# Kernel optimization log

Hardware: AMD Instinct MI355X
Metric: run time of the kernel (lower is better)

## Reference

```python
import jax, jax.numpy as jnp
import numpy as np

N, E, DIN, H, C, L = 100000, 1600000, 128, 128, 40, 4
EPS = 1e-5  # BatchNorm1d default eps


def _bn(x, g, b):
    # training-mode batchnorm over node dim, biased variance (PyTorch normalizes
    # the batch with biased var in forward)
    m = jnp.mean(x, axis=0)
    v = jnp.var(x, axis=0)
    return g * (x - m) * jax.lax.rsqrt(v + EPS) + b


def _sage(h, src, dst, Wl_i, bl_i, Wr_i):
    # PyG SAGEConv (aggr='mean', root_weight=True): lin_l(mean_j x_j) + lin_r(x_i)
    msg = h[src]                                             # [E, H]
    s = jax.ops.segment_sum(msg, dst, num_segments=N)        # [N, H]
    cnt = jax.ops.segment_sum(jnp.ones((E, 1), h.dtype), dst, num_segments=N)
    agg = s / jnp.maximum(cnt, 1.0)
    return agg @ Wl_i + bl_i + h @ Wr_i


def setup_inputs() -> dict:
    key = jax.random.key(0)
    ks = jax.random.split(key, 14)
    s = 0.05
    x = jax.random.normal(ks[0], (N, DIN), dtype=jnp.float32)
    edge_index = jax.random.randint(ks[1], (2, E), 0, N)
    return {
        "x": x,
        "W_in": jax.random.normal(ks[2], (DIN, H), dtype=jnp.float32) * s,
        "b_in": jnp.zeros((H,), jnp.float32),
        "g_in": jnp.ones((H,), jnp.float32),
        "beta_in": jnp.zeros((H,), jnp.float32),
        "Wl": jax.random.normal(ks[3], (L, H, H), dtype=jnp.float32) * s,
        "bl": jnp.zeros((L, H), jnp.float32),
        "Wr": jax.random.normal(ks[4], (L, H, H), dtype=jnp.float32) * s,
        "g_bn": jnp.ones((L, H), jnp.float32),
        "b_bn": jnp.zeros((L, H), jnp.float32),
        "W_out": jax.random.normal(ks[5], (H, C), dtype=jnp.float32) * s,
        "b_out": jnp.zeros((C,), jnp.float32),
        "edge_index": edge_index,
    }


def reference(x, W_in, b_in, g_in, beta_in, Wl, bl, Wr, g_bn, b_bn, W_out, b_out, edge_index):
    src, dst = edge_index[0], edge_index[1]
    h = jax.nn.relu(_bn(x @ W_in + b_in, g_in, beta_in))  # dropout p=0.0 -> identity
    for i in range(L):
        h = _sage(h, src, dst, Wl[i], bl[i], Wr[i])
        if i < L - 1:
            h = jax.nn.relu(_bn(h, g_bn[i], b_bn[i]))
    return h @ W_out + b_out
```

## Files before the change

### kernel.cpp

```cpp
#include <hip/hip_runtime.h>

#define N_NODES 100000
#define N_EDGES 1600000
#define HD 128
#define NLAYERS 4
#define COUT 40
#define BN_EPS 1e-5f
#define NBUCK 782
#define BUCK_CAP 3072
constexpr int GB = (N_NODES + 127) / 128;

typedef _Float16 half8 __attribute__((ext_vector_type(8)));
typedef float floatx4 __attribute__((ext_vector_type(4)));

__global__ void prep_kernel(const float* __restrict__ W_in,
                            const float* __restrict__ Wl,
                            const float* __restrict__ Wr,
                            const float* __restrict__ W_out,
                            _Float16* __restrict__ Wt_in,
                            _Float16* __restrict__ Wt_cat,
                            _Float16* __restrict__ Wt_out)
{
    int tid = blockIdx.x * blockDim.x + threadIdx.x;
    int stride = gridDim.x * blockDim.x;
    for (int idx = tid; idx < 128 * 128; idx += stride) {
        int n = idx >> 7, k = idx & 127;
        Wt_in[idx] = (_Float16)W_in[k * 128 + n];
    }
    for (int idx = tid; idx < 4 * 128 * 256; idx += stride) {
        int i = idx >> 15;
        int r = idx & 32767;
        int n = r >> 8, k = r & 255;
        Wt_cat[idx] = (_Float16)((k < 128) ? Wl[i * 16384 + k * 128 + n]
                                           : Wr[i * 16384 + (k - 128) * 128 + n]);
    }
    for (int idx = tid; idx < 48 * 128; idx += stride) {
        int n = idx >> 7, k = idx & 127;
        Wt_out[idx] = (n < COUT) ? (_Float16)W_out[k * COUT + n] : (_Float16)0.f;
    }
}

__global__ __launch_bounds__(256) void bucket_hist_kernel(const int* __restrict__ edst,
                                                          int* __restrict__ bcnt) {
    __shared__ int h[NBUCK];
    for (int b = threadIdx.x; b < NBUCK; b += 256) h[b] = 0;
    __syncthreads();
    int tid = blockIdx.x * 256 + threadIdx.x;
    int stride = gridDim.x * 256;
    for (int e = tid; e < N_EDGES; e += stride)
        atomicAdd(&h[edst[e] >> 7], 1);
    __syncthreads();
    for (int b = threadIdx.x; b < NBUCK; b += 256)
        if (h[b]) atomicAdd(&bcnt[b], h[b]);
}

__global__ void bucket_scan_kernel(const int* __restrict__ bcnt,
                                   int* __restrict__ bbase, int* __restrict__ bcur) {
    int lane = threadIdx.x;
    int run = 0;
    for (int base = 0; base < NBUCK; base += 64) {
        int i = base + lane;
        int orig = (i < NBUCK) ? bcnt[i] : 0;
        int v = orig;
        #pragma unroll
        for (int off = 1; off < 64; off <<= 1) {
            int t = __shfl_up(v, off);
            if (lane >= off) v += t;
        }
        int total = __shfl(v, 63);
        int excl = v - orig + run;
        if (i < NBUCK) { bbase[i] = excl; bcur[i] = excl; }
        run += total;
    }
    if (lane == 0) bbase[NBUCK] = run;
}

#define SCAT_T 16
__global__ __launch_bounds__(512) void bucket_scatter_kernel(const int* __restrict__ esrc,
                                                             const int* __restrict__ edst,
                                                             int* __restrict__ bcur,
                                                             int* __restrict__ bedges) {
    __shared__ int cnt[NBUCK], gpos[NBUCK];
    long base = (long)blockIdx.x * (512 * SCAT_T);
    for (int b = threadIdx.x; b < NBUCK; b += 512) cnt[b] = 0;
    __syncthreads();
    int srcs[SCAT_T], locs[SCAT_T], rnk[SCAT_T], bks[SCAT_T];
    #pragma unroll
    for (int j = 0; j < SCAT_T; ++j) {
        long e = base + j * 512 + threadIdx.x;
        if (e < N_EDGES) {
            int d = edst[e];
            srcs[j] = esrc[e];
            bks[j] = d >> 7;
            locs[j] = d & 127;
            rnk[j] = atomicAdd(&cnt[bks[j]], 1);
        } else bks[j] = -1;
    }
    __syncthreads();
    for (int b = threadIdx.x; b < NBUCK; b += 512) {
        int c = cnt[b];
        gpos[b] = c ? atomicAdd(&bcur[b], c) : 0;
    }
    __syncthreads();
    #pragma unroll
    for (int j = 0; j < SCAT_T; ++j)
        if (bks[j] >= 0)
            bedges[gpos[bks[j]] + rnk[j]] = (locs[j] << 17) | srcs[j];
}

__global__ __launch_bounds__(256) void bucket_sort_kernel(const int* __restrict__ bedges,
                                                          const int* __restrict__ bbase,
                                                          int* __restrict__ rs,
                                                          int* __restrict__ ssrc) {
    __shared__ int lsrc[BUCK_CAP];
    __shared__ int h[128], hin[128], lcur[128];
    int b = blockIdx.x;
    int s = bbase[b];
    int n = bbase[b + 1] - s;
    if (n > BUCK_CAP) n = BUCK_CAP;
    if (threadIdx.x < 128) h[threadIdx.x] = 0;
    __syncthreads();
    for (int i = threadIdx.x; i < n; i += 256) {
        int v = bedges[s + i];
        lsrc[i] = v;
        atomicAdd(&h[v >> 17], 1);
    }
    __syncthreads();
    if (threadIdx.x < 128) hin[threadIdx.x] = h[threadIdx.x];
    __syncthreads();
    #pragma unroll
    for (int off = 1; off < 128; off <<= 1) {
        int t = 0;
        if (threadIdx.x < 128 && (int)threadIdx.x >= off) t = h[threadIdx.x - off];
        __syncthreads();
        if (threadIdx.x < 128) h[threadIdx.x] += t;
        __syncthreads();
    }
    if (threadIdx.x < 128) {
        int excl = h[threadIdx.x] - hin[threadIdx.x];
        lcur[threadIdx.x] = excl;
        int node = b * 128 + threadIdx.x;
        if (node < N_NODES) rs[node] = s + excl;
    }
    if (b == NBUCK - 1 && threadIdx.x == 0) rs[N_NODES] = bbase[NBUCK];
    __syncthreads();
    for (int i = threadIdx.x; i < n; i += 256) {
        int v = lsrc[i];
        int r = atomicAdd(&lcur[v >> 17], 1);
        ssrc[s + r] = v & 0x1FFFF;
    }
}

__global__ __launch_bounds__(256) void aggregate_kernel(const _Float16* __restrict__ H,
                                                        const int* __restrict__ rs,
                                                        const int* __restrict__ ssrc,
                                                        _Float16* __restrict__ AGG) {
    int wid = (blockIdx.x * 256 + threadIdx.x) >> 6;
    int lane = threadIdx.x & 63;
    int grp = lane >> 4, l16 = lane & 15;
    int dst = wid * 4 + grp;
    int e0 = rs[dst], e1 = rs[dst + 1];
    int deg = e1 - e0;

    half8 acca = {0, 0, 0, 0, 0, 0, 0, 0};
    half8 accb = {0, 0, 0, 0, 0, 0, 0, 0};
    const _Float16* __restrict__ Hc = H + l16 * 8;

    int e = e0;
    for (; e + 4 <= e1; e += 4) {
        int s0 = ssrc[e], s1 = ssrc[e + 1], s2 = ssrc[e + 2], s3 = ssrc[e + 3];
        half8 v0 = *(const half8*)(Hc + (long)s0 * HD);
        half8 v1 = *(const half8*)(Hc + (long)s1 * HD);
        half8 v2 = *(const half8*)(Hc + (long)s2 * HD);
        half8 v3 = *(const half8*)(Hc + (long)s3 * HD);
        acca += v0 + v1;
        accb += v2 + v3;
    }
    for (; e < e1; ++e) {
        half8 v0 = *(const half8*)(Hc + (long)ssrc[e] * HD);
        acca += v0;
    }
    half8 acc = acca + accb;
    _Float16 inv = (_Float16)(1.f / (float)max(deg, 1));
    acc *= inv;
    *(half8*)(AGG + (long)dst * HD + l16 * 8) = acc;
}

template <int CT, int KS, bool HAS_A1, bool A_F32, bool OUT_F32, bool STATS>
__global__ __launch_bounds__(256, 2) void gemm_kernel(const void* __restrict__ A0v,
                                                      const _Float16* __restrict__ A1,
                                                      const _Float16* __restrict__ Wt,
                                                      const float* __restrict__ bias,
                                                      void* __restrict__ Yv,
                                                      int out_stride, int ncols,
                                                      float* __restrict__ gstats) {
    constexpr int K = KS * 32;
    constexpr int KSC = (KS > 4) ? 4 : KS;
    __shared__ _Float16 bsm[KSC * 32 * CT * 16];
    int wave = threadIdx.x >> 6;
    int lane = threadIdx.x & 63;
    int quad = lane >> 4;
    int l16 = lane & 15;
    int row_base = (blockIdx.x * 4 + wave) * 32;
    bool active = row_base < N_NODES;

    floatx4 acc[2][CT];
    #pragma unroll
    for (int rt = 0; rt < 2; ++rt)
        #pragma unroll
        for (int c = 0; c < CT; ++c)
            acc[rt][c] = (floatx4){0.f, 0.f, 0.f, 0.f};

    for (int ch = 0; ch < KS; ch += KSC) {
        if (ch) __syncthreads();
        for (int i = threadIdx.x; i < KSC * CT * 64; i += 256) {
            int n = i % (CT * 16);
            int ko = i / (CT * 16);
            half8 v = *(const half8*)(Wt + n * K + (ch * 4 + ko) * 8);
            int slot = (((ko >> 2) * CT + (n >> 4)) * 4 + (ko & 3)) * 16 + (n & 15);
            *(half8*)(bsm + slot * 8) = v;
        }
        __syncthreads();
        if (active) {
            #pragma unroll
            for (int s2 = 0; s2 < KSC; ++s2) {
                int s = ch + s2;
                int kk = s * 32 + quad * 8;
                half8 afrag[2];
                #pragma unroll
                for (int rt = 0; rt < 2; ++rt) {
                    int r = row_base + rt * 16 + l16;
                    if (r > N_NODES - 1) r = N_NODES - 1;
                    if (A_F32) {
                        const float* p = (const float*)A0v + (long)r * 128 + kk;
                        floatx4 f0 = *(const floatx4*)p;
                        floatx4 f1 = *(const floatx4*)(p + 4);
                        #pragma unroll
                        for (int j = 0; j < 4; ++j) {
                            afrag[rt][j]     = (_Float16)f0[j];
                            afrag[rt][4 + j] = (_Float16)f1[j];
                        }
                    } else {
                        const _Float16* p;
                        if (HAS_A1 && kk >= 128) p = A1 + (long)r * 128 + (kk - 128);
                        else                     p = (const _Float16*)A0v + (long)r * 128 + kk;
                        afrag[rt] = *(const half8*)p;
                    }
                }
                #pragma unroll
                for (int c = 0; c < CT; ++c) {
                    half8 bfrag = *(const half8*)(bsm + ((s2 * CT + c) * 64 + lane) * 8);
                    #pragma unroll
                    for (int rt = 0; rt < 2; ++rt)
                        acc[rt][c] = __builtin_amdgcn_mfma_f32_16x16x32_f16(afrag[rt], bfrag, acc[rt][c], 0, 0, 0);
                }
            }
        }
    }

    float* lsum = (float*)bsm;
    float* lsq  = lsum + 128;
    if (STATS) {
        __syncthreads();
        if (threadIdx.x < 128) { lsum[threadIdx.x] = 0.f; lsq[threadIdx.x] = 0.f; }
        __syncthreads();
    } else {
        if (!active) return;
    }

    #pragma unroll
    for (int c = 0; c < CT; ++c) {
        int col = c * 16 + l16;
        float s_c = 0.f, q_c = 0.f;
        if (active && col < ncols) {
            float bv = bias[col];
            #pragma unroll
            for (int rt = 0; rt < 2; ++rt) {
                #pragma unroll
                for (int i = 0; i < 4; ++i) {
                    int r = row_base + rt * 16 + quad * 4 + i;
                    if (r < N_NODES) {
                        float v = acc[rt][c][i] + bv;
                        if (OUT_F32) ((float*)Yv)[(long)r * out_stride + col] = v;
                        else         ((_Float16*)Yv)[(long)r * out_stride + col] = (_Float16)v;
                        if (STATS) { s_c += v; q_c += v * v; }
                    }
                }
            }
        }
        if (STATS) {
            s_c += __shfl_xor(s_c, 16); s_c += __shfl_xor(s_c, 32);
            q_c += __shfl_xor(q_c, 16); q_c += __shfl_xor(q_c, 32);
            if (lane < 16 && active) {
                atomicAdd(&lsum[col], s_c);
                atomicAdd(&lsq[col], q_c);
            }
        }
    }

    if (STATS) {
        __syncthreads();
        if (threadIdx.x < 128) {
            atomicAdd(&gstats[threadIdx.x], lsum[threadIdx.x]);
            atomicAdd(&gstats[128 + threadIdx.x], lsq[threadIdx.x]);
        }
    }
}

__global__ __launch_bounds__(256) void bn_apply_kernel(const _Float16* __restrict__ Y,
                                                       const float* __restrict__ gstats,
                                                       const float* __restrict__ g,
                                                       const float* __restrict__ b,
                                                       _Float16* __restrict__ H) {
    __shared__ float sc[128], sh[128];
    if (threadIdx.x < 128) {
        int col = threadIdx.x;
        float m = gstats[col] * (1.f / (float)N_NODES);
        float v = gstats[128 + col] * (1.f / (float)N_NODES) - m * m;
        float s = g[col] * rsqrtf(v + BN_EPS);
        sc[col] = s;
        sh[col] = b[col] - m * s;
    }
    __syncthreads();
    long total = (long)N_NODES * HD / 8;
    for (long t = (long)blockIdx.x * blockDim.x + threadIdx.x; t < total;
         t += (long)gridDim.x * blockDim.x) {
        long base = t * 8;
        int col0 = (int)(base & 127);
        half8 in = *(const half8*)(Y + base);
        half8 outv;
        #pragma unroll
        for (int j = 0; j < 8; ++j) {
            float v = (float)in[j];
            float r = v * sc[col0 + j] + sh[col0 + j];
            outv[j] = (_Float16)fmaxf(r, 0.f);
        }
        *(half8*)(H + base) = outv;
    }
}

extern "C" void kernel_launch(void* const* d_in, const int* in_sizes, int n_in,
                              void* d_out, int out_size, void* d_ws, size_t ws_size,
                              hipStream_t stream) {
    (void)in_sizes; (void)n_in; (void)out_size; (void)ws_size;
    const float* x       = (const float*)d_in[0];
    const float* W_in    = (const float*)d_in[1];
    const float* b_in    = (const float*)d_in[2];
    const float* g_in    = (const float*)d_in[3];
    const float* beta_in = (const float*)d_in[4];
    const float* Wl      = (const float*)d_in[5];
    const float* bl      = (const float*)d_in[6];
    const float* Wr      = (const float*)d_in[7];
    const float* g_bn    = (const float*)d_in[8];
    const float* b_bn    = (const float*)d_in[9];
    const float* W_out   = (const float*)d_in[10];
    const float* b_out   = (const float*)d_in[11];
    const int*   ei      = (const int*)d_in[12];
    const int* esrc = ei;
    const int* edst = ei + N_EDGES;
    float* out = (float*)d_out;

    char* w = (char*)d_ws;
    auto alloc = [&](size_t bytes) -> char* {
        char* p = w; w += (bytes + 255) & ~(size_t)255; return p;
    };
    int* rs           = (int*)alloc((N_NODES + 1) * sizeof(int));
    int* bcnt         = (int*)alloc((NBUCK + 1) * sizeof(int));
    int* bbase        = (int*)alloc((NBUCK + 1) * sizeof(int));
    int* bcur         = (int*)alloc(NBUCK * sizeof(int));
    int* ssrc         = (int*)alloc(N_EDGES * sizeof(int));
    _Float16* Wt_in   = (_Float16*)alloc(128 * 128 * 2);
    _Float16* Wt_cat  = (_Float16*)alloc(4 * 128 * 256 * 2);
    _Float16* Wt_out  = (_Float16*)alloc(48 * 128 * 2);
    _Float16* hbuf    = (_Float16*)alloc((size_t)N_NODES * HD * 2);
    _Float16* agg     = (_Float16*)alloc((size_t)N_NODES * HD * 2);
    _Float16* ybuf    = (_Float16*)alloc((size_t)N_NODES * HD * 2);
    float* gstats     = (float*)alloc(4 * 256 * 4);
    int* bedges       = (int*)agg;

    hipMemsetAsync(bcnt, 0, (NBUCK + 1) * sizeof(int), stream);
    hipMemsetAsync(gstats, 0, 4 * 256 * 4, stream);
    prep_kernel<<<256, 256, 0, stream>>>(W_in, Wl, Wr, W_out, Wt_in, Wt_cat, Wt_out);
    bucket_hist_kernel<<<64, 256, 0, stream>>>(edst, bcnt);
    bucket_scan_kernel<<<1, 64, 0, stream>>>(bcnt, bbase, bcur);
    bucket_scatter_kernel<<<(N_EDGES + 8191) / 8192, 512, 0, stream>>>(esrc, edst, bcur, bedges);
    bucket_sort_kernel<<<NBUCK, 256, 0, stream>>>(bedges, bbase, rs, ssrc);

    gemm_kernel<8, 4, false, true, false, true><<<GB, 256, 0, stream>>>(
        x, nullptr, Wt_in, b_in, ybuf, HD, HD, gstats);
    bn_apply_kernel<<<1600, 256, 0, stream>>>(ybuf, gstats, g_in, beta_in, hbuf);

    for (int i = 0; i < NLAYERS; ++i) {
        aggregate_kernel<<<N_NODES / 16, 256, 0, stream>>>(hbuf, rs, ssrc, agg);
        if (i < NLAYERS - 1) {
            float* gs = gstats + (i + 1) * 256;
            gemm_kernel<8, 8, true, false, false, true><<<GB, 256, 0, stream>>>(
                agg, hbuf, Wt_cat + i * 128 * 256, bl + i * 128, ybuf, HD, HD, gs);
            bn_apply_kernel<<<1600, 256, 0, stream>>>(ybuf, gs, g_bn + i * 128, b_bn + i * 128, hbuf);
        } else {
            gemm_kernel<8, 8, true, false, false, false><<<GB, 256, 0, stream>>>(
                agg, hbuf, Wt_cat + i * 128 * 256, bl + i * 128, ybuf, HD, HD, nullptr);
        }
    }

    gemm_kernel<3, 4, false, false, true, false><<<GB, 256, 0, stream>>>(
        ybuf, nullptr, Wt_out, b_out, out, COUT, COUT, nullptr);
}
```

Baseline: 651.0 us.

## Fuse BatchNorm+ReLU into aggregate gather and GEMM A-operand loads

Removes the separate bn_apply pass by storing pre-normalization outputs and applying per-column scale/shift plus ReLU inside the aggregate kernel's gathers and the GEMM's root-feature fragment loads. This drops a full read-and-write pass over the 100000x128 fp16 activations per layer. In exchange, normalization is recomputed for every gathered edge (16x per node on average), and the scale/shift are held in fp16 rather than fp32. It also ping-pongs two activation buffers so the GEMM can read the previous layer's output while writing the next.

```diff
diff --git a/kernel.cpp b/kernel.cpp
--- a/kernel.cpp
+++ b/kernel.cpp
@@ -12,6 +12,12 @@
 
 typedef _Float16 half8 __attribute__((ext_vector_type(8)));
 typedef float floatx4 __attribute__((ext_vector_type(4)));
+
+__device__ __forceinline__ half8 bnrelu8(half8 v, half8 s, half8 h) {
+    half8 t = s * v + h;
+    half8 z = {0, 0, 0, 0, 0, 0, 0, 0};
+    return __builtin_elementwise_max(t, z);
+}
 
 __global__ void prep_kernel(const float* __restrict__ W_in,
                             const float* __restrict__ Wl,
@@ -151,10 +157,24 @@
     }
 }
 
-__global__ __launch_bounds__(256) void aggregate_kernel(const _Float16* __restrict__ H,
+__global__ __launch_bounds__(256) void aggregate_kernel(const _Float16* __restrict__ Y,
                                                         const int* __restrict__ rs,
                                                         const int* __restrict__ ssrc,
+                                                        const float* __restrict__ gstats,
+                                                        const float* __restrict__ g,
+                                                        const float* __restrict__ b,
                                                         _Float16* __restrict__ AGG) {
+    __shared__ _Float16 sc16[128], sh16[128];
+    if (threadIdx.x < 128) {
+        int col = threadIdx.x;
+        float m = gstats[col] * (1.f / (float)N_NODES);
+        float v = gstats[128 + col] * (1.f / (float)N_NODES) - m * m;
+        float s = g[col] * rsqrtf(v + BN_EPS);
+        sc16[col] = (_Float16)s;
+        sh16[col] = (_Float16)(b[col] - m * s);
+    }
+    __syncthreads();
+
     int wid = (blockIdx.x * 256 + threadIdx.x) >> 6;
     int lane = threadIdx.x & 63;
     int grp = lane >> 4, l16 = lane & 15;
@@ -162,23 +182,25 @@
     int e0 = rs[dst], e1 = rs[dst + 1];
     int deg = e1 - e0;
 
+    half8 scv = *(const half8*)(sc16 + l16 * 8);
+    half8 shv = *(const half8*)(sh16 + l16 * 8);
     half8 acca = {0, 0, 0, 0, 0, 0, 0, 0};
     half8 accb = {0, 0, 0, 0, 0, 0, 0, 0};
-    const _Float16* __restrict__ Hc = H + l16 * 8;
+    const _Float16* __restrict__ Yc = Y + l16 * 8;
 
     int e = e0;
     for (; e + 4 <= e1; e += 4) {
         int s0 = ssrc[e], s1 = ssrc[e + 1], s2 = ssrc[e + 2], s3 = ssrc[e + 3];
-        half8 v0 = *(const half8*)(Hc + (long)s0 * HD);
-        half8 v1 = *(const half8*)(Hc + (long)s1 * HD);
-        half8 v2 = *(const half8*)(Hc + (long)s2 * HD);
-        half8 v3 = *(const half8*)(Hc + (long)s3 * HD);
-        acca += v0 + v1;
-        accb += v2 + v3;
+        half8 v0 = *(const half8*)(Yc + (long)s0 * HD);
+        half8 v1 = *(const half8*)(Yc + (long)s1 * HD);
+        half8 v2 = *(const half8*)(Yc + (long)s2 * HD);
+        half8 v3 = *(const half8*)(Yc + (long)s3 * HD);
+        acca += bnrelu8(v0, scv, shv) + bnrelu8(v1, scv, shv);
+        accb += bnrelu8(v2, scv, shv) + bnrelu8(v3, scv, shv);
     }
     for (; e < e1; ++e) {
-        half8 v0 = *(const half8*)(Hc + (long)ssrc[e] * HD);
-        acca += v0;
+        half8 v0 = *(const half8*)(Yc + (long)ssrc[e] * HD);
+        acca += bnrelu8(v0, scv, shv);
     }
     half8 acc = acca + accb;
     _Float16 inv = (_Float16)(1.f / (float)max(deg, 1));
@@ -186,23 +208,38 @@
     *(half8*)(AGG + (long)dst * HD + l16 * 8) = acc;
 }
 
-template <int CT, int KS, bool HAS_A1, bool A_F32, bool OUT_F32, bool STATS>
+template <int CT, int KS, bool HAS_A1, bool A_F32, bool OUT_F32, bool STATS, bool BN_A1>
 __global__ __launch_bounds__(256, 2) void gemm_kernel(const void* __restrict__ A0v,
                                                       const _Float16* __restrict__ A1,
                                                       const _Float16* __restrict__ Wt,
                                                       const float* __restrict__ bias,
                                                       void* __restrict__ Yv,
                                                       int out_stride, int ncols,
-                                                      float* __restrict__ gstats) {
+                                                      float* __restrict__ gstats_out,
+                                                      const float* __restrict__ bn_stats,
+                                                      const float* __restrict__ bn_g,
+                                                      const float* __restrict__ bn_b) {
     constexpr int K = KS * 32;
     constexpr int KSC = (KS > 4) ? 4 : KS;
     __shared__ _Float16 bsm[KSC * 32 * CT * 16];
+    __shared__ _Float16 a1sc[128], a1sh[128];
     int wave = threadIdx.x >> 6;
     int lane = threadIdx.x & 63;
     int quad = lane >> 4;
     int l16 = lane & 15;
     int row_base = (blockIdx.x * 4 + wave) * 32;
     bool active = row_base < N_NODES;
+
+    if (BN_A1) {
+        if (threadIdx.x < 128) {
+            int col = threadIdx.x;
+            float m = bn_stats[col] * (1.f / (float)N_NODES);
+            float v = bn_stats[128 + col] * (1.f / (float)N_NODES) - m * m;
+            float s = bn_g[col] * rsqrtf(v + BN_EPS);
+            a1sc[col] = (_Float16)s;
+            a1sh[col] = (_Float16)(bn_b[col] - m * s);
+        }
+    }
 
     floatx4 acc[2][CT];
     #pragma unroll
@@ -226,6 +263,7 @@
             for (int s2 = 0; s2 < KSC; ++s2) {
                 int s = ch + s2;
                 int kk = s * 32 + quad * 8;
+                bool fromA1 = HAS_A1 && (kk >= 128);
                 half8 afrag[2];
                 #pragma unroll
                 for (int rt = 0; rt < 2; ++rt) {
@@ -242,9 +280,14 @@
                         }
                     } else {
                         const _Float16* p;
-                        if (HAS_A1 && kk >= 128) p = A1 + (long)r * 128 + (kk - 128);
-                        else                     p = (const _Float16*)A0v + (long)r * 128 + kk;
+                        if (fromA1) p = A1 + (long)r * 128 + (kk - 128);
+                        else        p = (const _Float16*)A0v + (long)r * 128 + kk;
                         afrag[rt] = *(const half8*)p;
+                        if (BN_A1 && fromA1) {
+                            half8 s8 = *(const half8*)(a1sc + (kk - 128));
+                            half8 h8 = *(const half8*)(a1sh + (kk - 128));
+                            afrag[rt] = bnrelu8(afrag[rt], s8, h8);
+                        }
                     }
                 }
                 #pragma unroll
@@ -301,41 +344,9 @@
     if (STATS) {
         __syncthreads();
         if (threadIdx.x < 128) {
-            atomicAdd(&gstats[threadIdx.x], lsum[threadIdx.x]);
-            atomicAdd(&gstats[128 + threadIdx.x], lsq[threadIdx.x]);
-        }
-    }
-}
-
-__global__ __launch_bounds__(256) void bn_apply_kernel(const _Float16* __restrict__ Y,
-                                                       const float* __restrict__ gstats,
-                                                       const float* __restrict__ g,
-                                                       const float* __restrict__ b,
-                                                       _Float16* __restrict__ H) {
-    __shared__ float sc[128], sh[128];
-    if (threadIdx.x < 128) {
-        int col = threadIdx.x;
-        float m = gstats[col] * (1.f / (float)N_NODES);
-        float v = gstats[128 + col] * (1.f / (float)N_NODES) - m * m;
-        float s = g[col] * rsqrtf(v + BN_EPS);
-        sc[col] = s;
-        sh[col] = b[col] - m * s;
-    }
-    __syncthreads();
-    long total = (long)N_NODES * HD / 8;
-    for (long t = (long)blockIdx.x * blockDim.x + threadIdx.x; t < total;
-         t += (long)gridDim.x * blockDim.x) {
-        long base = t * 8;
-        int col0 = (int)(base & 127);
-        half8 in = *(const half8*)(Y + base);
-        half8 outv;
-        #pragma unroll
-        for (int j = 0; j < 8; ++j) {
-            float v = (float)in[j];
-            float r = v * sc[col0 + j] + sh[col0 + j];
-            outv[j] = (_Float16)fmaxf(r, 0.f);
-        }
-        *(half8*)(H + base) = outv;
+            atomicAdd(&gstats_out[threadIdx.x], lsum[threadIdx.x]);
+            atomicAdd(&gstats_out[128 + threadIdx.x], lsq[threadIdx.x]);
+        }
     }
 }
 
@@ -372,9 +383,9 @@
     _Float16* Wt_in   = (_Float16*)alloc(128 * 128 * 2);
     _Float16* Wt_cat  = (_Float16*)alloc(4 * 128 * 256 * 2);
     _Float16* Wt_out  = (_Float16*)alloc(48 * 128 * 2);
-    _Float16* hbuf    = (_Float16*)alloc((size_t)N_NODES * HD * 2);
+    _Float16* ybufA   = (_Float16*)alloc((size_t)N_NODES * HD * 2);
+    _Float16* ybufB   = (_Float16*)alloc((size_t)N_NODES * HD * 2);
     _Float16* agg     = (_Float16*)alloc((size_t)N_NODES * HD * 2);
-    _Float16* ybuf    = (_Float16*)alloc((size_t)N_NODES * HD * 2);
     float* gstats     = (float*)alloc(4 * 256 * 4);
     int* bedges       = (int*)agg;
 
@@ -386,23 +397,28 @@
     bucket_scatter_kernel<<<(N_EDGES + 8191) / 8192, 512, 0, stream>>>(esrc, edst, bcur, bedges);
     bucket_sort_kernel<<<NBUCK, 256, 0, stream>>>(bedges, bbase, rs, ssrc);
 
-    gemm_kernel<8, 4, false, true, false, true><<<GB, 256, 0, stream>>>(
-        x, nullptr, Wt_in, b_in, ybuf, HD, HD, gstats);
-    bn_apply_kernel<<<1600, 256, 0, stream>>>(ybuf, gstats, g_in, beta_in, hbuf);
-
+    gemm_kernel<8, 4, false, true, false, true, false><<<GB, 256, 0, stream>>>(
+        x, nullptr, Wt_in, b_in, ybufA, HD, HD, gstats, nullptr, nullptr, nullptr);
+
+    _Float16* cur = ybufA;
+    _Float16* nxt = ybufB;
     for (int i = 0; i < NLAYERS; ++i) {
-        aggregate_kernel<<<N_NODES / 16, 256, 0, stream>>>(hbuf, rs, ssrc, agg);
+        const float* gs   = gstats + i * 256;
+        const float* bn_g = (i == 0) ? g_in    : g_bn + (i - 1) * 128;
+        const float* bn_b = (i == 0) ? beta_in : b_bn + (i - 1) * 128;
+        aggregate_kernel<<<N_NODES / 16, 256, 0, stream>>>(cur, rs, ssrc, gs, bn_g, bn_b, agg);
         if (i < NLAYERS - 1) {
-            float* gs = gstats + (i + 1) * 256;
-            gemm_kernel<8, 8, true, false, false, true><<<GB, 256, 0, stream>>>(
-                agg, hbuf, Wt_cat + i * 128 * 256, bl + i * 128, ybuf, HD, HD, gs);
-            bn_apply_kernel<<<1600, 256, 0, stream>>>(ybuf, gs, g_bn + i * 128, b_bn + i * 128, hbuf);
+            gemm_kernel<8, 8, true, false, false, true, true><<<GB, 256, 0, stream>>>(
+                agg, cur, Wt_cat + i * 128 * 256, bl + i * 128, nxt, HD, HD,
+                gstats + (i + 1) * 256, gs, bn_g, bn_b);
         } else {
-            gemm_kernel<8, 8, true, false, false, false><<<GB, 256, 0, stream>>>(
-                agg, hbuf, Wt_cat + i * 128 * 256, bl + i * 128, ybuf, HD, HD, nullptr);
-        }
-    }
-
-    gemm_kernel<3, 4, false, false, true, false><<<GB, 256, 0, stream>>>(
-        ybuf, nullptr, Wt_out, b_out, out, COUT, COUT, nullptr);
-}
+            gemm_kernel<8, 8, true, false, false, false, true><<<GB, 256, 0, stream>>>(
+                agg, cur, Wt_cat + i * 128 * 256, bl + i * 128, nxt, HD, HD,
+                nullptr, gs, bn_g, bn_b);
+        }
+        _Float16* t = cur; cur = nxt; nxt = t;
+    }
+
+    gemm_kernel<3, 4, false, false, true, false, false><<<GB, 256, 0, stream>>>(
+        cur, nullptr, Wt_out, b_out, out, COUT, COUT, nullptr, nullptr, nullptr, nullptr);
+}
```

After: 625.9 us. 1.04x faster.
